# Kernel tuning notes

Measured on AMD Instinct MI355X. Metric: run time of the kernel, lower is better.

Reference implementation:

```python
import jax, jax.numpy as jnp
import numpy as np

M = 2  # sqrt(n_heads)

def setup_inputs() -> dict:
    key = jax.random.key(0)
    k1, k2, k3 = jax.random.split(key, 3)
    b, H, W, c = 8, 256, 256, 64
    x = jax.random.normal(k1, (b, H, W, c), dtype=jnp.float32)
    # 1x1 conv weights expressed as matrices: qkv [c, 3c], project [c, c]
    scale = 1.0 / np.sqrt(c)
    Wqkv = jax.random.normal(k2, (c, 3 * c), dtype=jnp.float32) * scale
    Wproj = jax.random.normal(k3, (c, c), dtype=jnp.float32) * scale
    return {"x": x, "Wqkv": Wqkv, "Wproj": Wproj}


def reference(x, Wqkv, Wproj):
    b, H, W, c = x.shape
    h, w = H // M, W // M
    temp = c ** (-0.5)  # n_features ** -0.5
    # 1x1 conv qkv projection (bias-free)
    qkv = jnp.einsum('byxc,cd->byxd', x, Wqkv)  # [b,H,W,3c]
    q, k, v = jnp.split(qkv, 3, axis=-1)

    def blk(t):
        # 'b (h m1) (w m2) c -> b (m1 m2) c (h w)'
        t = t.reshape(b, h, M, w, M, c)
        t = t.transpose(0, 2, 4, 5, 1, 3)  # b m1 m2 c h w
        return t.reshape(b, M * M, c, h * w)

    q, k, v = blk(q), blk(k), blk(v)
    # channel-attention: c x c score per block, contracted over hw
    score = jnp.einsum('bncl,bndl->bncd', q, k) * temp
    weight = jax.nn.softmax(score, axis=-1)
    out = jnp.einsum('bncd,bndl->bncl', weight, v)
    # inverse rearrange: 'b (m1 m2) c (h w) -> b (h m1) (w m2) c'
    out = out.reshape(b, M, M, c, h, w).transpose(0, 4, 1, 5, 2, 3).reshape(b, H, W, c)
    # 1x1 conv output projection
    return jnp.einsum('byxc,cd->byxd', out, Wproj)
```

## Files before the change

kernel.cpp:

```cpp
#include <hip/hip_runtime.h>

typedef float f32x4 __attribute__((ext_vector_type(4)));
typedef __bf16 bf16x8 __attribute__((ext_vector_type(8)));
typedef short s16x8 __attribute__((ext_vector_type(8)));

__device__ __forceinline__ unsigned short f2bf(float f) {
  unsigned u = __builtin_bit_cast(unsigned, f);
  return (unsigned short)((u + 0x7fffu + ((u >> 16) & 1u)) >> 16);
}
__device__ __forceinline__ float bf2f(unsigned short s) {
  unsigned u = ((unsigned)s) << 16;
  return __builtin_bit_cast(float, u);
}

#define PSTR 136

__global__ __launch_bounds__(256) void gram_kernel(const float* __restrict__ x,
                                                   float* __restrict__ G) {
  __shared__ unsigned short xsh[64 * PSTR];
  __shared__ unsigned short xsl[64 * PSTR];
  const int tid = threadIdx.x;
  const int lane = tid & 63;
  const int wave = tid >> 6;
  const int blk = blockIdx.x;
  const int chunk = blk & 31;
  const int bn = blk >> 5;
  const int b = bn >> 2;
  const int m1 = (bn >> 1) & 1;
  const int m2 = bn & 1;
  const int p0 = (tid & 63) * 2;
  const int c0 = (tid >> 6) * 16;
  const int xx = 2 * p0 + m2;
  const int mrow = lane & 15;
  const int k8 = (lane >> 4) * 8;
  const int tr0 = (wave >> 1) * 2;
  const int tc0 = (wave & 1) * 2;

  f32x4 acc[2][2];
#pragma unroll
  for (int i = 0; i < 2; ++i)
#pragma unroll
    for (int j = 0; j < 2; ++j) acc[i][j] = (f32x4){0.f, 0.f, 0.f, 0.f};

  f32x4 v[8];
  {
    int y = 2 * (chunk * 4) + m1;
    const float* p = x + ((b * 256 + y) * 256 + xx) * 64 + c0;
#pragma unroll
    for (int i = 0; i < 4; ++i) {
      v[i] = ((const f32x4*)p)[i];
      v[4 + i] = ((const f32x4*)(p + 128))[i];
    }
  }

#pragma unroll
  for (int round = 0; round < 4; ++round) {
    __syncthreads();
#pragma unroll
    for (int i = 0; i < 16; ++i) {
      float f0 = v[i >> 2][i & 3];
      float f1 = v[4 + (i >> 2)][i & 3];
      unsigned short h0 = f2bf(f0), h1 = f2bf(f1);
      unsigned short g0 = f2bf(f0 - bf2f(h0)), g1 = f2bf(f1 - bf2f(h1));
      *(unsigned*)&xsh[(c0 + i) * PSTR + p0] = (unsigned)h0 | ((unsigned)h1 << 16);
      *(unsigned*)&xsl[(c0 + i) * PSTR + p0] = (unsigned)g0 | ((unsigned)g1 << 16);
    }
    __syncthreads();
    if (round < 3) {
      int y = 2 * (chunk * 4 + round + 1) + m1;
      const float* p = x + ((b * 256 + y) * 256 + xx) * 64 + c0;
#pragma unroll
      for (int i = 0; i < 4; ++i) {
        v[i] = ((const f32x4*)p)[i];
        v[4 + i] = ((const f32x4*)(p + 128))[i];
      }
    }
#pragma unroll
    for (int kst = 0; kst < 4; ++kst) {
      s16x8 rh[2], rl[2], qh[2], ql[2];
#pragma unroll
      for (int i = 0; i < 2; ++i) {
        rh[i] = *(const s16x8*)&xsh[(16 * (tr0 + i) + mrow) * PSTR + kst * 32 + k8];
        rl[i] = *(const s16x8*)&xsl[(16 * (tr0 + i) + mrow) * PSTR + kst * 32 + k8];
        qh[i] = *(const s16x8*)&xsh[(16 * (tc0 + i) + mrow) * PSTR + kst * 32 + k8];
        ql[i] = *(const s16x8*)&xsl[(16 * (tc0 + i) + mrow) * PSTR + kst * 32 + k8];
      }
#pragma unroll
      for (int i = 0; i < 2; ++i)
#pragma unroll
        for (int j = 0; j < 2; ++j) {
          bf16x8 ah = __builtin_bit_cast(bf16x8, rh[i]);
          bf16x8 al = __builtin_bit_cast(bf16x8, rl[i]);
          bf16x8 bh = __builtin_bit_cast(bf16x8, qh[j]);
          bf16x8 bl = __builtin_bit_cast(bf16x8, ql[j]);
          acc[i][j] = __builtin_amdgcn_mfma_f32_16x16x32_bf16(ah, bh, acc[i][j], 0, 0, 0);
          acc[i][j] = __builtin_amdgcn_mfma_f32_16x16x32_bf16(ah, bl, acc[i][j], 0, 0, 0);
          acc[i][j] = __builtin_amdgcn_mfma_f32_16x16x32_bf16(al, bh, acc[i][j], 0, 0, 0);
        }
    }
  }
  float* Gp = G + bn * 4096;
#pragma unroll
  for (int i = 0; i < 2; ++i)
#pragma unroll
    for (int j = 0; j < 2; ++j)
#pragma unroll
      for (int r = 0; r < 4; ++r) {
        int row = 16 * (tr0 + i) + (lane >> 4) * 4 + r;
        int col = 16 * (tc0 + j) + (lane & 15);
        atomicAdd(&Gp[row * 64 + col], acc[i][j][r]);
      }
}

__device__ __forceinline__ void mm64(const float* Ab, int ars, int acs,
                                     const float* Bb, float* Dst, int ds,
                                     float scale, int ti4, int tj4) {
  float acc[4][4] = {};
  for (int kk = 0; kk < 64; ++kk) {
    float av[4];
#pragma unroll
    for (int i = 0; i < 4; ++i) av[i] = Ab[(ti4 + i) * ars + kk * acs];
#pragma unroll
    for (int j = 0; j < 4; ++j) {
      float bv = Bb[kk * 68 + tj4 + j];
#pragma unroll
      for (int i = 0; i < 4; ++i) acc[i][j] += av[i] * bv;
    }
  }
#pragma unroll
  for (int i = 0; i < 4; ++i)
#pragma unroll
    for (int j = 0; j < 4; ++j) Dst[(ti4 + i) * ds + tj4 + j] = scale * acc[i][j];
}

__global__ __launch_bounds__(256) void fuse_kernel(const float* __restrict__ G,
                                                   const float* __restrict__ Wqkv,
                                                   const float* __restrict__ Wproj,
                                                   unsigned short* __restrict__ Fh,
                                                   unsigned short* __restrict__ Fl) {
  __shared__ float A[64 * 68];
  __shared__ float B[64 * 68];
  __shared__ float T[64 * 68];
  const int tid = threadIdx.x;
  const int bn = blockIdx.x;
  const int ti4 = (tid >> 4) * 4, tj4 = (tid & 15) * 4;

  for (int i = tid; i < 4096; i += 256) {
    int r = i >> 6, c = i & 63;
    A[r * 68 + c] = G[bn * 4096 + i];
    B[r * 68 + c] = Wqkv[r * 192 + 64 + c];
  }
  __syncthreads();
  mm64(A, 68, 1, B, T, 68, 1.f, ti4, tj4);
  __syncthreads();
  for (int i = tid; i < 4096; i += 256) {
    int r = i >> 6, c = i & 63;
    B[r * 68 + c] = Wqkv[r * 192 + c];
  }
  __syncthreads();
  mm64(B, 1, 68, T, A, 68, 0.125f, ti4, tj4);
  __syncthreads();
  if (tid < 64) {
    float mx = -1e30f;
    for (int d = 0; d < 64; ++d) mx = fmaxf(mx, A[tid * 68 + d]);
    float s = 0.f;
    for (int d = 0; d < 64; ++d) {
      float e = __expf(A[tid * 68 + d] - mx);
      A[tid * 68 + d] = e;
      s += e;
    }
    float inv = 1.f / s;
    for (int d = 0; d < 64; ++d) A[tid * 68 + d] *= inv;
  }
  __syncthreads();
  for (int i = tid; i < 4096; i += 256) {
    int r = i >> 6, c = i & 63;
    B[r * 68 + c] = Wproj[i];
  }
  __syncthreads();
  mm64(A, 1, 68, B, T, 68, 1.f, ti4, tj4);
  __syncthreads();
  for (int i = tid; i < 4096; i += 256) {
    int r = i >> 6, c = i & 63;
    B[r * 68 + c] = Wqkv[r * 192 + 128 + c];
  }
  __syncthreads();
  mm64(B, 68, 1, T, A, 68, 1.f, ti4, tj4);
  __syncthreads();
  for (int i = tid; i < 4096; i += 256) {
    int f = i & 63, e = i >> 6;
    float val = A[f * 68 + e];
    unsigned short h = f2bf(val);
    Fh[bn * 4096 + e * 64 + f] = h;
    Fl[bn * 4096 + e * 64 + f] = f2bf(val - bf2f(h));
  }
}

__global__ __launch_bounds__(256) void out_kernel(const float* __restrict__ x,
                                                  const unsigned short* __restrict__ Fh,
                                                  const unsigned short* __restrict__ Fl,
                                                  float* __restrict__ out) {
  const int tid = threadIdx.x;
  const int lane = tid & 63;
  const int wave = tid >> 6;
  const int blk = blockIdx.x;
  const int hyg = blk & 63;
  const int bn = blk >> 6;
  const int b = bn >> 2;
  const int m1 = (bn >> 1) & 1;
  const int m2 = bn & 1;

  s16x8 bh[2][4], bl[2][4];
  {
    const unsigned short* Fhp = Fh + bn * 4096;
    const unsigned short* Flp = Fl + bn * 4096;
    const int e = lane & 15;
    const int k0 = (lane >> 4) * 8;
#pragma unroll
    for (int ksj = 0; ksj < 2; ++ksj)
#pragma unroll
      for (int tc = 0; tc < 4; ++tc) {
        int off = (tc * 16 + e) * 64 + ksj * 32 + k0;
        bh[ksj][tc] = *(const s16x8*)&Fhp[off];
        bl[ksj][tc] = *(const s16x8*)&Flp[off];
      }
  }

  for (int r = 0; r < 2; ++r) {
    int hy = hyg * 2 + r;
    int y = 2 * hy + m1;
    const float* xrow = x + ((b * 256 + y) * 256) * 64;
    float* orow = out + ((b * 256 + y) * 256) * 64;
#pragma unroll
    for (int ptI = 0; ptI < 2; ++ptI) {
      int pt = wave + ptI * 4;
      int wx = pt * 16 + (lane & 15);
      int xx = 2 * wx + m2;
      const float* pp = xrow + xx * 64 + (lane >> 4) * 8;
      s16x8 ah[2], al[2];
#pragma unroll
      for (int ksj = 0; ksj < 2; ++ksj) {
        f32x4 u0 = *(const f32x4*)(pp + ksj * 32);
        f32x4 u1 = *(const f32x4*)(pp + ksj * 32 + 4);
        s16x8 hv, lv;
#pragma unroll
        for (int j = 0; j < 4; ++j) {
          unsigned short hb0 = f2bf(u0[j]);
          unsigned short hb1 = f2bf(u1[j]);
          hv[j] = (short)hb0;
          hv[4 + j] = (short)hb1;
          lv[j] = (short)f2bf(u0[j] - bf2f(hb0));
          lv[4 + j] = (short)f2bf(u1[j] - bf2f(hb1));
        }
        ah[ksj] = hv;
        al[ksj] = lv;
      }
      f32x4 acc[4];
#pragma unroll
      for (int tc = 0; tc < 4; ++tc) acc[tc] = (f32x4){0.f, 0.f, 0.f, 0.f};
#pragma unroll
      for (int ksj = 0; ksj < 2; ++ksj)
#pragma unroll
        for (int tc = 0; tc < 4; ++tc) {
          bf16x8 A_h = __builtin_bit_cast(bf16x8, ah[ksj]);
          bf16x8 A_l = __builtin_bit_cast(bf16x8, al[ksj]);
          bf16x8 B_h = __builtin_bit_cast(bf16x8, bh[ksj][tc]);
          bf16x8 B_l = __builtin_bit_cast(bf16x8, bl[ksj][tc]);
          acc[tc] = __builtin_amdgcn_mfma_f32_16x16x32_bf16(A_h, B_h, acc[tc], 0, 0, 0);
          acc[tc] = __builtin_amdgcn_mfma_f32_16x16x32_bf16(A_h, B_l, acc[tc], 0, 0, 0);
          acc[tc] = __builtin_amdgcn_mfma_f32_16x16x32_bf16(A_l, B_h, acc[tc], 0, 0, 0);
        }
#pragma unroll
      for (int tc = 0; tc < 4; ++tc)
#pragma unroll
        for (int j = 0; j < 4; ++j) {
          int prow = (lane >> 4) * 4 + j;
          int xx2 = 2 * (pt * 16 + prow) + m2;
          orow[xx2 * 64 + tc * 16 + (lane & 15)] = acc[tc][j];
        }
    }
  }
}

extern "C" void kernel_launch(void* const* d_in, const int* in_sizes, int n_in,
                              void* d_out, int out_size, void* d_ws, size_t ws_size,
                              hipStream_t stream) {
  (void)in_sizes; (void)n_in; (void)out_size; (void)ws_size;
  const float* x = (const float*)d_in[0];
  const float* Wqkv = (const float*)d_in[1];
  const float* Wproj = (const float*)d_in[2];
  float* out = (float*)d_out;
  float* G = (float*)d_ws;
  unsigned short* Fh = (unsigned short*)(G + 32 * 4096);
  unsigned short* Fl = Fh + 32 * 4096;

  hipMemsetAsync(G, 0, 32 * 4096 * sizeof(float), stream);
  gram_kernel<<<1024, 256, 0, stream>>>(x, G);
  fuse_kernel<<<32, 256, 0, stream>>>(G, Wqkv, Wproj, Fh, Fl);
  out_kernel<<<2048, 256, 0, stream>>>(x, Fh, Fl, out);
}
```

Before: 294.3 us.

## Replace Gram atomics with per-chunk partials reduced in fuse kernel

The gram kernel now writes each block's 64x64 partial Gram matrix to its own slot instead of atomically adding into a shared per-(batch,block) matrix, which also removes the memset launch. The fuse kernel sums the 32 partials with vectorized loads before its matmuls. The softmax is spread across all 256 threads with a shared-memory reduction, and the small matmul loop gets an unroll hint. This trades atomic contention and an extra launch for a larger workspace (32x more G storage) and extra global reads in the single-wave-per-CU fuse kernel.

```diff
diff --git a/kernel.cpp b/kernel.cpp
--- a/kernel.cpp
+++ b/kernel.cpp
@@ -99,7 +99,7 @@
         }
     }
   }
-  float* Gp = G + bn * 4096;
+  float* Gp = G + (bn * 32 + chunk) * 4096;
 #pragma unroll
   for (int i = 0; i < 2; ++i)
 #pragma unroll
@@ -108,7 +108,7 @@
       for (int r = 0; r < 4; ++r) {
         int row = 16 * (tr0 + i) + (lane >> 4) * 4 + r;
         int col = 16 * (tc0 + j) + (lane & 15);
-        atomicAdd(&Gp[row * 64 + col], acc[i][j][r]);
+        Gp[row * 64 + col] = acc[i][j][r];
       }
 }
 
@@ -116,6 +116,7 @@
                                      const float* Bb, float* Dst, int ds,
                                      float scale, int ti4, int tj4) {
   float acc[4][4] = {};
+#pragma unroll 4
   for (int kk = 0; kk < 64; ++kk) {
     float av[4];
 #pragma unroll
@@ -141,13 +142,24 @@
   __shared__ float A[64 * 68];
   __shared__ float B[64 * 68];
   __shared__ float T[64 * 68];
+  __shared__ float red[256];
   const int tid = threadIdx.x;
   const int bn = blockIdx.x;
   const int ti4 = (tid >> 4) * 4, tj4 = (tid & 15) * 4;
 
+  {
+    const float* Gp = G + bn * 32 * 4096;
+#pragma unroll
+    for (int pass = 0; pass < 4; ++pass) {
+      int i = (pass * 256 + tid) * 4;
+      f32x4 s = (f32x4){0.f, 0.f, 0.f, 0.f};
+#pragma unroll
+      for (int c2 = 0; c2 < 32; ++c2) s += *(const f32x4*)&Gp[c2 * 4096 + i];
+      *(f32x4*)&A[(i >> 6) * 68 + (i & 63)] = s;
+    }
+  }
   for (int i = tid; i < 4096; i += 256) {
     int r = i >> 6, c = i & 63;
-    A[r * 68 + c] = G[bn * 4096 + i];
     B[r * 68 + c] = Wqkv[r * 192 + 64 + c];
   }
   __syncthreads();
@@ -160,19 +172,29 @@
   __syncthreads();
   mm64(B, 1, 68, T, A, 68, 0.125f, ti4, tj4);
   __syncthreads();
-  if (tid < 64) {
+  {
+    const int row = tid >> 2, q = (tid & 3) * 16;
     float mx = -1e30f;
-    for (int d = 0; d < 64; ++d) mx = fmaxf(mx, A[tid * 68 + d]);
+#pragma unroll
+    for (int d = 0; d < 16; ++d) mx = fmaxf(mx, A[row * 68 + q + d]);
+    red[tid] = mx;
+    __syncthreads();
+    mx = fmaxf(fmaxf(red[row * 4], red[row * 4 + 1]),
+               fmaxf(red[row * 4 + 2], red[row * 4 + 3]));
     float s = 0.f;
-    for (int d = 0; d < 64; ++d) {
-      float e = __expf(A[tid * 68 + d] - mx);
-      A[tid * 68 + d] = e;
+#pragma unroll
+    for (int d = 0; d < 16; ++d) {
+      float e = __expf(A[row * 68 + q + d] - mx);
+      A[row * 68 + q + d] = e;
       s += e;
     }
-    float inv = 1.f / s;
-    for (int d = 0; d < 64; ++d) A[tid * 68 + d] *= inv;
-  }
-  __syncthreads();
+    __syncthreads();
+    red[tid] = s;
+    __syncthreads();
+    float inv = 1.f / (red[row * 4] + red[row * 4 + 1] + red[row * 4 + 2] + red[row * 4 + 3]);
+#pragma unroll
+    for (int d = 0; d < 16; ++d) A[row * 68 + q + d] *= inv;
+  }
   for (int i = tid; i < 4096; i += 256) {
     int r = i >> 6, c = i & 63;
     B[r * 68 + c] = Wproj[i];
@@ -291,10 +313,9 @@
   const float* Wproj = (const float*)d_in[2];
   float* out = (float*)d_out;
   float* G = (float*)d_ws;
-  unsigned short* Fh = (unsigned short*)(G + 32 * 4096);
+  unsigned short* Fh = (unsigned short*)(G + 32 * 32 * 4096);
   unsigned short* Fl = Fh + 32 * 4096;
 
-  hipMemsetAsync(G, 0, 32 * 4096 * sizeof(float), stream);
   gram_kernel<<<1024, 256, 0, stream>>>(x, G);
   fuse_kernel<<<32, 256, 0, stream>>>(G, Wqkv, Wproj, Fh, Fl);
   out_kernel<<<2048, 256, 0, stream>>>(x, Fh, Fl, out);
```

Result: slower. 302.3 us (+2.7%).
